# Kernel tuning notes

Measured on AMD Instinct MI355X. Metric: run time of the kernel, lower is better.

The kernel has to match this reference:

```python
import jax, jax.numpy as jnp
import numpy as np

B, N, C = 4, 2048, 1024
H = 16
D = C // H  # head_size = 64


def setup_inputs() -> dict:
    key = jax.random.key(0)
    ks = jax.random.split(key, 9)
    s = 1.0 / np.sqrt(C)
    return {
        "x": jax.random.normal(ks[0], (B, N, C), dtype=jnp.float32),
        "Wq": jax.random.normal(ks[1], (C, C), dtype=jnp.float32) * s,
        "bq": jnp.zeros((C,), dtype=jnp.float32),
        "Wk": jax.random.normal(ks[2], (C, C), dtype=jnp.float32) * s,
        "bk": jnp.zeros((C,), dtype=jnp.float32),
        "Wv": jax.random.normal(ks[3], (C, C), dtype=jnp.float32) * s,
        "bv": jnp.zeros((C,), dtype=jnp.float32),
        "Wo": jax.random.normal(ks[4], (C, C), dtype=jnp.float32) * s,
        "bo": jnp.zeros((C,), dtype=jnp.float32),
    }


def reference(x, Wq, bq, Wk, bk, Wv, bv, Wo, bo):
    scale = 1.0 / np.sqrt(D).astype(np.float32)
    # projections: [B,N,C] -> [B,H,N,D]
    def split_heads(t):
        return t.reshape(B, N, H, D).transpose(0, 2, 1, 3)
    q = split_heads(x @ Wq + bq)
    k = split_heads(x @ Wk + bk)
    v = split_heads(x @ Wv + bv)
    # scores: [B,H,N,N] -- full NxN materialized as in the original module
    attn = jnp.einsum("bhqd,bhkd->bhqk", q, k) * scale
    attn = jax.nn.softmax(attn, axis=-1)
    # context: [B,H,N,D] -> [B,N,C]
    ctx = jnp.einsum("bhqk,bhkd->bhqd", attn, v)
    ctx = ctx.transpose(0, 2, 1, 3).reshape(B, N, C)
    return ctx @ Wo + bo
```

## Files before the change

### kernel.cpp

```cpp
#include <hip/hip_runtime.h>
#include <hip/hip_bf16.h>

typedef __bf16 bf16_t;
typedef __bf16 bf16x4 __attribute__((ext_vector_type(4)));
typedef __bf16 bf16x8 __attribute__((ext_vector_type(8)));
typedef float f32x4 __attribute__((ext_vector_type(4)));
typedef unsigned int u32;

#define B_ 4
#define N_ 2048
#define C_ 1024
#define H_ 16
#define D_ 64

#define MFMA32(a, b, c) __builtin_amdgcn_mfma_f32_16x16x32_bf16((a), (b), (c), 0, 0, 0)

#if __has_builtin(__builtin_amdgcn_exp2f)
#define EXP2F(x) __builtin_amdgcn_exp2f(x)
#else
#define EXP2F(x) __expf((x) * 0.6931471805599453f)
#endif

#define QSCALE 0.18033688011112042f

__device__ __forceinline__ void async16(const bf16_t* g, bf16_t* l) {
    __builtin_amdgcn_global_load_lds(
        (const u32 __attribute__((address_space(1)))*)g,
        (u32 __attribute__((address_space(3)))*)l, 16, 0, 0);
}

#define SBAR()  asm volatile("s_barrier" ::: "memory")
#define VM6()   asm volatile("s_waitcnt vmcnt(6)" ::: "memory")
#define VM0()   asm volatile("s_waitcnt vmcnt(0)" ::: "memory")

__global__ __launch_bounds__(256)
void xconv_kernel(const float* __restrict__ x, bf16_t* __restrict__ xb)
{
    const size_t i = ((size_t)blockIdx.x * 256 + threadIdx.x) * 8;
    float4 a = *(const float4*)(x + i);
    float4 b = *(const float4*)(x + i + 4);
    bf16x8 o;
    o[0] = (bf16_t)a.x; o[1] = (bf16_t)a.y; o[2] = (bf16_t)a.z; o[3] = (bf16_t)a.w;
    o[4] = (bf16_t)b.x; o[5] = (bf16_t)b.y; o[6] = (bf16_t)b.z; o[7] = (bf16_t)b.w;
    *(bf16x8*)(xb + i) = o;
}

__global__ __launch_bounds__(256)
void wtrans_kernel(const float* __restrict__ W0, const float* __restrict__ W1,
                   const float* __restrict__ W2, const float* __restrict__ W3,
                   bf16_t* __restrict__ T0, bf16_t* __restrict__ T1,
                   bf16_t* __restrict__ T2, bf16_t* __restrict__ T3)
{
    const float* W; bf16_t* T;
    switch (blockIdx.z) {
        case 0:  W = W0; T = T0; break;
        case 1:  W = W1; T = T1; break;
        case 2:  W = W2; T = T2; break;
        default: W = W3; T = T3; break;
    }
    __shared__ bf16_t tile[64 * 72];
    const int tid = threadIdx.x;
    const int r0 = blockIdx.y * 64;
    const int c0 = blockIdx.x * 64;

    const int rr = tid >> 4;
    const int cc = (tid & 15) * 4;
    #pragma unroll
    for (int i = 0; i < 4; ++i) {
        const int row = rr + i * 16;
        float4 v = *(const float4*)(W + (size_t)(r0 + row) * C_ + c0 + cc);
        tile[(cc + 0) * 72 + row] = (bf16_t)v.x;
        tile[(cc + 1) * 72 + row] = (bf16_t)v.y;
        tile[(cc + 2) * 72 + row] = (bf16_t)v.z;
        tile[(cc + 3) * 72 + row] = (bf16_t)v.w;
    }
    __syncthreads();
    #pragma unroll
    for (int i = 0; i < 2; ++i) {
        const int ch = i * 256 + tid;
        const int n  = ch >> 3;
        const int k8 = (ch & 7) * 8;
        bf16x8 o = *(const bf16x8*)&tile[n * 72 + k8];
        *(bf16x8*)(T + (size_t)(c0 + n) * C_ + r0 + k8) = o;
    }
}

__device__ __forceinline__ void gemm128x256(const bf16_t* __restrict__ A,
                                            const bf16_t* __restrict__ Bt,
                                            bf16_t* smem, int m0, int n0,
                                            f32x4 (&acc)[4][4])
{
    const int tid  = threadIdx.x;
    const int w    = tid >> 6;
    const int lane = tid & 63;
    const int c    = lane & 15;
    const int quad = lane >> 4;
    const int wr   = w >> 2;
    const int wc   = w & 3;

    const int r0s = tid >> 2;
    const int kc  = (tid & 3) ^ ((r0s >> 1) & 3);
    const bf16_t* Ast0 = A  + (size_t)(m0 + r0s) * C_ + kc * 8;
    const bf16_t* Bst0 = Bt + (size_t)(n0 + r0s) * C_ + kc * 8;
    const bf16_t* Bst1 = Bt + (size_t)(n0 + r0s + 128) * C_ + kc * 8;

    const int xorc = (quad ^ ((c >> 1) & 3)) * 8;
    const bf16_t* Ard = smem + (wr * 64 + c) * 32 + xorc;
    const bf16_t* Brd = smem + 24576 + (wc * 64 + c) * 32 + xorc;
    bf16_t* sw = smem + w * 512;

    bf16x8 af[2][4], bfv[2][4];

#define STAGE6(BUF, KOFF) do { \
    async16(Ast0 + (KOFF),      sw + (BUF) * 8192); \
    async16(Ast0 + (KOFF) + 32, sw + (BUF) * 8192 + 4096); \
    async16(Bst0 + (KOFF),      sw + 24576 + (BUF) * 16384); \
    async16(Bst1 + (KOFF),      sw + 24576 + (BUF) * 16384 + 4096); \
    async16(Bst0 + (KOFF) + 32, sw + 24576 + (BUF) * 16384 + 8192); \
    async16(Bst1 + (KOFF) + 32, sw + 24576 + (BUF) * 16384 + 12288); } while (0)

#define LDFRAGS16(BUF) do { \
    _Pragma("unroll") \
    for (int ks = 0; ks < 2; ++ks) { \
        _Pragma("unroll") \
        for (int i = 0; i < 4; ++i) \
            af[ks][i]  = *(const bf16x8*)(Ard + (BUF) * 8192 + ks * 4096 + i * 512); \
        _Pragma("unroll") \
        for (int j = 0; j < 4; ++j) \
            bfv[ks][j] = *(const bf16x8*)(Brd + (BUF) * 16384 + ks * 8192 + j * 512); \
    } } while (0)

#define MFMA32ALL() do { \
    _Pragma("unroll") \
    for (int ks = 0; ks < 2; ++ks) \
        _Pragma("unroll") \
        for (int i = 0; i < 4; ++i) \
            _Pragma("unroll") \
            for (int j = 0; j < 4; ++j) \
                acc[i][j] = MFMA32(af[ks][i], bfv[ks][j], acc[i][j]); } while (0)

#define TILE(BUF, NXT, DOSTAGE, KOFF, VMK) do { \
    if (DOSTAGE) STAGE6(NXT, KOFF); \
    LDFRAGS16(BUF); \
    __builtin_amdgcn_s_setprio(1); MFMA32ALL(); __builtin_amdgcn_s_setprio(0); \
    VMK; \
    SBAR(); \
} while (0)

    STAGE6(0, 0);
    STAGE6(1, 64);
    VM6();
    SBAR();

    #pragma unroll 1
    for (int tt = 0; tt < 4; ++tt) {
        TILE(0, 2, 1, 128, VM6());
        TILE(1, 0, 1, 192, VM6());
        TILE(2, 1, 1, 256, VM6());
        Ast0 += 192; Bst0 += 192; Bst1 += 192;
    }
    TILE(0, 2, 1, 128, VM6());
    TILE(1, 0, 1, 192, VM6());
    TILE(2, 1, 0, 0,   VM0());
    TILE(0, 0, 0, 0,   ((void)0));

#undef TILE
#undef MFMA32ALL
#undef LDFRAGS16
#undef STAGE6
}

__global__ __launch_bounds__(512)
void gemm_qkv_kernel(const bf16_t* __restrict__ A, const bf16_t* __restrict__ Wt,
                     const float* __restrict__ bq, const float* __restrict__ bk,
                     const float* __restrict__ bv,
                     bf16_t* __restrict__ Qb, bf16_t* __restrict__ Kb,
                     bf16_t* __restrict__ Vtb)
{
    __shared__ bf16_t smem[73728];

    const int bid = blockIdx.x;
    const int x8  = bid & 7;
    const int ii  = bid >> 3;
    const int mb  = x8 * 8 + (ii & 7);
    const int nb  = ii >> 3;
    const int m0  = mb * 128, n0 = nb * 256;

    f32x4 acc[4][4] = {};
    gemm128x256(A, Wt, smem, m0, n0, acc);

    const int tid  = threadIdx.x;
    const int w    = tid >> 6;
    const int lane = tid & 63;
    const int c    = lane & 15;
    const int quad = lane >> 4;
    const int wr   = w >> 2;
    const int wc   = w & 3;

    const int which = n0 >> 10;
    const float* bias = (which == 0) ? bq : (which == 1) ? bk : bv;

    #pragma unroll
    for (int nf = 0; nf < 4; ++nf) {
        const int col  = n0 + wc * 64 + nf * 16 + c;
        const int ncol = col & 1023;
        const float bsf = bias[ncol];
        const int h = ncol >> 6, d = ncol & 63;
        #pragma unroll
        for (int mf = 0; mf < 4; ++mf) {
            const int rbase = m0 + wr * 64 + mf * 16 + quad * 4;
            if (which < 2) {
                bf16_t* out = which ? Kb : Qb;
                const float sc = which ? 1.0f : QSCALE;
                #pragma unroll
                for (int r = 0; r < 4; ++r) {
                    const int row = rbase + r;
                    const int bb = row >> 11, n = row & 2047;
                    out[(((size_t)bb * H_ + h) * N_ + n) * D_ + d] =
                        (bf16_t)((acc[mf][nf][r] + bsf) * sc);
                }
            } else {
                const int bb = rbase >> 11, nbv = rbase & 2047;
                bf16x4 o;
                #pragma unroll
                for (int r = 0; r < 4; ++r) o[r] = (bf16_t)(acc[mf][nf][r] + bsf);
                *(bf16x4*)(Vtb + (((size_t)bb * H_ + h) * D_ + d) * N_ + nbv) = o;
            }
        }
    }
}

__global__ __launch_bounds__(512)
void gemm_out_kernel(const bf16_t* __restrict__ A, const bf16_t* __restrict__ Bt,
                     const float* __restrict__ bias, float* __restrict__ out)
{
    __shared__ bf16_t smem[73728];

    const int bid = blockIdx.x;
    const int x8  = bid & 7;
    const int ii  = bid >> 3;
    const int mb  = x8 * 8 + (ii & 7);
    const int nb  = ii >> 3;
    const int m0  = mb * 128, n0 = nb * 256;

    f32x4 acc[4][4] = {};
    gemm128x256(A, Bt, smem, m0, n0, acc);

    const int tid  = threadIdx.x;
    const int w    = tid >> 6;
    const int lane = tid & 63;
    const int c    = lane & 15;
    const int quad = lane >> 4;
    const int wr   = w >> 2;
    const int wc   = w & 3;

    #pragma unroll
    for (int nf = 0; nf < 4; ++nf) {
        const int col   = n0 + wc * 64 + nf * 16 + c;
        const float bsf = bias[col];
        #pragma unroll
        for (int mf = 0; mf < 4; ++mf) {
            const int rbase = m0 + wr * 64 + mf * 16 + quad * 4;
            #pragma unroll
            for (int r = 0; r < 4; ++r)
                out[(size_t)(rbase + r) * C_ + col] = acc[mf][nf][r] + bsf;
        }
    }
}

__global__ __launch_bounds__(256, 2)
void attn_kernel(const bf16_t* __restrict__ Q, const bf16_t* __restrict__ K,
                 const bf16_t* __restrict__ Vt, bf16_t* __restrict__ ctx)
{
    __shared__ bf16_t ksh[64 * 64];
    __shared__ bf16_t vsh[64 * 64];

    const int tid  = threadIdx.x;
    const int w    = tid >> 6;
    const int lane = tid & 63;
    const int c    = lane & 15;
    const int quad = lane >> 4;

    const int bid   = blockIdx.x;
    const int bh    = (bid & 7) * 8 + ((bid >> 3) & 7);
    const int qtile = bid >> 6;
    const int b = bh >> 4, h = bh & 15;
    const size_t base = (size_t)bh * N_ * D_;
    const int qb = qtile * 256 + w * 64;

    bf16x8 qf[4][2];
    #pragma unroll
    for (int g = 0; g < 4; ++g)
        #pragma unroll
        for (int hh = 0; hh < 2; ++hh)
            qf[g][hh] = *(const bf16x8*)(Q + base + (size_t)(qb + g * 16 + c) * D_ + hh * 32 + quad * 8);

    bf16x8 ones;
    #pragma unroll
    for (int j = 0; j < 8; ++j) ones[j] = (bf16_t)1.0f;

    f32x4 O[4][4] = {};
    f32x4 O5[4] = {};

    for (int kt = 0; kt < N_; kt += 64) {
        __syncthreads();
        #pragma unroll
        for (int ph = 0; ph < 2; ++ph) {
            const int ch = ph * 256 + tid;
            const int rr = ch >> 3;
            const int e8 = ch & 7;
            const int sw = (e8 ^ (rr & 7)) * 8;
            bf16x8 kv = *(const bf16x8*)(K  + base + (size_t)(kt + rr) * D_ + e8 * 8);
            *(bf16x8*)&ksh[rr * 64 + sw] = kv;
            bf16x8 vv = *(const bf16x8*)(Vt + base + (size_t)rr * N_ + kt + e8 * 8);
            *(bf16x8*)&vsh[rr * 64 + sw] = vv;
        }
        __syncthreads();

        #pragma unroll
        for (int ss = 0; ss < 2; ++ss) {
            bf16x8 kb[2][2];
            #pragma unroll
            for (int s2 = 0; s2 < 2; ++s2) {
                const int key = (ss * 2 + s2) * 16 + c;
                #pragma unroll
                for (int hh = 0; hh < 2; ++hh)
                    kb[s2][hh] = *(const bf16x8*)&ksh[key * 64 + (((hh * 4 + quad) ^ (c & 7)) * 8)];
            }
            bf16x8 va[4];
            const int k8lo = ss * 4 + (quad >> 1);
            const int half = (quad & 1) * 4;
            #pragma unroll
            for (int df = 0; df < 4; ++df) {
                const int row = (df * 16 + c) * 64;
                bf16x4 lo = *(const bf16x4*)&vsh[row + ((k8lo       ^ (c & 7)) * 8) + half];
                bf16x4 hi = *(const bf16x4*)&vsh[row + (((k8lo + 2) ^ (c & 7)) * 8) + half];
                #pragma unroll
                for (int j = 0; j < 4; ++j) { va[df][j] = lo[j]; va[df][4 + j] = hi[j]; }
            }

            #pragma unroll
            for (int g = 0; g < 4; ++g) {
                f32x4 s0 = {}, s1 = {};
                s0 = MFMA32(kb[0][0], qf[g][0], s0);
                s0 = MFMA32(kb[0][1], qf[g][1], s0);
                s1 = MFMA32(kb[1][0], qf[g][0], s1);
                s1 = MFMA32(kb[1][1], qf[g][1], s1);

                bf16x8 pb;
                #pragma unroll
                for (int r = 0; r < 4; ++r) {
                    pb[r]     = (bf16_t)EXP2F(s0[r]);
                    pb[4 + r] = (bf16_t)EXP2F(s1[r]);
                }

                #pragma unroll
                for (int df = 0; df < 4; ++df)
                    O[g][df] = MFMA32(va[df], pb, O[g][df]);
                O5[g] = MFMA32(ones, pb, O5[g]);
            }
        }
    }

    #pragma unroll
    for (int g = 0; g < 4; ++g) {
        const float inv_l = 1.0f / O5[g][0];
        const int q = qb + g * 16 + c;
        #pragma unroll
        for (int df = 0; df < 4; ++df) {
            bf16x4 o;
            #pragma unroll
            for (int r = 0; r < 4; ++r) o[r] = (bf16_t)(O[g][df][r] * inv_l);
            *(bf16x4*)(ctx + ((size_t)b * N_ + q) * C_ + h * 64 + df * 16 + quad * 4) = o;
        }
    }
}

extern "C" void kernel_launch(void* const* d_in, const int* in_sizes, int n_in,
                              void* d_out, int out_size, void* d_ws, size_t ws_size,
                              hipStream_t stream) {
    const float* x  = (const float*)d_in[0];
    const float* Wq = (const float*)d_in[1];
    const float* bq = (const float*)d_in[2];
    const float* Wk = (const float*)d_in[3];
    const float* bk = (const float*)d_in[4];
    const float* Wv = (const float*)d_in[5];
    const float* bv = (const float*)d_in[6];
    const float* Wo = (const float*)d_in[7];
    const float* bo = (const float*)d_in[8];

    bf16_t* ws = (bf16_t*)d_ws;
    const size_t per = (size_t)B_ * N_ * C_;
    bf16_t* xb  = ws;
    bf16_t* ctx = ws;
    bf16_t* Qb  = ws + per;
    bf16_t* Kb  = ws + 2 * per;
    bf16_t* Vtb = ws + 3 * per;
    bf16_t* Wtqkv = ws + 4 * per;
    bf16_t* Wtq = Wtqkv;
    bf16_t* Wtk = Wtqkv + (size_t)C_ * C_;
    bf16_t* Wtv = Wtqkv + 2 * (size_t)C_ * C_;
    bf16_t* Wto = Wtqkv + 3 * (size_t)C_ * C_;

    dim3 blk(256);

    xconv_kernel<<<dim3(per / 2048), blk, 0, stream>>>(x, xb);
    wtrans_kernel<<<dim3(16, 16, 4), blk, 0, stream>>>(Wq, Wk, Wv, Wo, Wtq, Wtk, Wtv, Wto);

    gemm_qkv_kernel<<<dim3(768), dim3(512), 0, stream>>>(xb, Wtqkv, bq, bk, bv, Qb, Kb, Vtb);

    attn_kernel<<<dim3(512), blk, 0, stream>>>(Qb, Kb, Vtb, ctx);

    gemm_out_kernel<<<dim3(256), dim3(512), 0, stream>>>(ctx, Wto, bo, (float*)d_out);
}
```

Baseline: 252.1 us.

## Triple-buffer K/V tiles with async global-to-LDS loads in attention kernel

Replaces the synchronous per-tile K/V load into shared memory (two barriers per tile) with a three-stage ring buffer filled by global_load_lds async copies, so each tile's load overlaps the compute of earlier tiles and only one barrier per tile is needed. The row-sum MFMA against a ones vector is replaced by a scalar accumulation of the exponentials plus a cross-lane shuffle reduction at the end. MFMA sections are wrapped in s_setprio to favour matrix issue. LDS use grows to 48 KB per block, which may limit occupancy, and correctness depends on the hand-placed vmcnt waits and the unrolled loop covering all 32 tiles.

```diff
diff --git a/kernel.cpp b/kernel.cpp
--- a/kernel.cpp
+++ b/kernel.cpp
@@ -31,6 +31,7 @@
 
 #define SBAR()  asm volatile("s_barrier" ::: "memory")
 #define VM6()   asm volatile("s_waitcnt vmcnt(6)" ::: "memory")
+#define VM4()   asm volatile("s_waitcnt vmcnt(4)" ::: "memory")
 #define VM0()   asm volatile("s_waitcnt vmcnt(0)" ::: "memory")
 
 __global__ __launch_bounds__(256)
@@ -272,8 +273,7 @@
 void attn_kernel(const bf16_t* __restrict__ Q, const bf16_t* __restrict__ K,
                  const bf16_t* __restrict__ Vt, bf16_t* __restrict__ ctx)
 {
-    __shared__ bf16_t ksh[64 * 64];
-    __shared__ bf16_t vsh[64 * 64];
+    __shared__ bf16_t smem[24576];
 
     const int tid  = threadIdx.x;
     const int w    = tid >> 6;
@@ -288,6 +288,82 @@
     const size_t base = (size_t)bh * N_ * D_;
     const int qb = qtile * 256 + w * 64;
 
+    const int rs  = tid >> 3;
+    const int kcs = (tid & 7) ^ (rs & 7);
+    const bf16_t* Kst = K  + base + (size_t)rs * 64 + kcs * 8;
+    const bf16_t* Vst = Vt + base + (size_t)rs * 2048 + kcs * 8;
+    bf16_t* dstK = smem + w * 512;
+    bf16_t* dstV = smem + 12288 + w * 512;
+
+#define ASTAGE(NXT, T) do { \
+    async16(Kst + (T) * 4096,         dstK + (NXT) * 4096); \
+    async16(Kst + (T) * 4096 + 2048,  dstK + (NXT) * 4096 + 2048); \
+    async16(Vst + (T) * 64,           dstV + (NXT) * 4096); \
+    async16(Vst + (T) * 64 + 65536,   dstV + (NXT) * 4096 + 2048); } while (0)
+
+#define COMPUTE(BUF) do { \
+    const bf16_t* ksh = smem + (BUF) * 4096; \
+    const bf16_t* vsh = smem + 12288 + (BUF) * 4096; \
+    _Pragma("unroll") \
+    for (int ss = 0; ss < 2; ++ss) { \
+        bf16x8 kb[2][2]; \
+        _Pragma("unroll") \
+        for (int s2 = 0; s2 < 2; ++s2) { \
+            const int key = (ss * 2 + s2) * 16 + c; \
+            _Pragma("unroll") \
+            for (int hh = 0; hh < 2; ++hh) \
+                kb[s2][hh] = *(const bf16x8*)&ksh[key * 64 + (((hh * 4 + quad) ^ (c & 7)) * 8)]; \
+        } \
+        bf16x8 va[4]; \
+        const int k8lo = ss * 4 + (quad >> 1); \
+        const int half = (quad & 1) * 4; \
+        _Pragma("unroll") \
+        for (int df = 0; df < 4; ++df) { \
+            const int row = (df * 16 + c) * 64; \
+            bf16x4 lo = *(const bf16x4*)&vsh[row + ((k8lo       ^ (c & 7)) * 8) + half]; \
+            bf16x4 hi = *(const bf16x4*)&vsh[row + (((k8lo + 2) ^ (c & 7)) * 8) + half]; \
+            _Pragma("unroll") \
+            for (int j = 0; j < 4; ++j) { va[df][j] = lo[j]; va[df][4 + j] = hi[j]; } \
+        } \
+        _Pragma("unroll") \
+        for (int g = 0; g < 4; ++g) { \
+            f32x4 s0 = {}, s1 = {}; \
+            __builtin_amdgcn_s_setprio(1); \
+            s0 = MFMA32(kb[0][0], qf[g][0], s0); \
+            s0 = MFMA32(kb[0][1], qf[g][1], s0); \
+            s1 = MFMA32(kb[1][0], qf[g][0], s1); \
+            s1 = MFMA32(kb[1][1], qf[g][1], s1); \
+            __builtin_amdgcn_s_setprio(0); \
+            bf16x8 pb; \
+            float ls = 0.0f; \
+            _Pragma("unroll") \
+            for (int r = 0; r < 4; ++r) { \
+                const float e0 = EXP2F(s0[r]); \
+                const float e1 = EXP2F(s1[r]); \
+                pb[r]     = (bf16_t)e0; \
+                pb[4 + r] = (bf16_t)e1; \
+                ls += e0 + e1; \
+            } \
+            lsum[g] += ls; \
+            __builtin_amdgcn_s_setprio(1); \
+            _Pragma("unroll") \
+            for (int df = 0; df < 4; ++df) \
+                O[g][df] = MFMA32(va[df], pb, O[g][df]); \
+            __builtin_amdgcn_s_setprio(0); \
+        } \
+    } \
+} while (0)
+
+#define ATILE(BUF, NXT, DOSTAGE, TREL, VMK) do { \
+    if (DOSTAGE) ASTAGE(NXT, TREL); \
+    COMPUTE(BUF); \
+    VMK; \
+    SBAR(); \
+} while (0)
+
+    ASTAGE(0, 0);
+    ASTAGE(1, 1);
+
     bf16x8 qf[4][2];
     #pragma unroll
     for (int g = 0; g < 4; ++g)
@@ -295,76 +371,32 @@
         for (int hh = 0; hh < 2; ++hh)
             qf[g][hh] = *(const bf16x8*)(Q + base + (size_t)(qb + g * 16 + c) * D_ + hh * 32 + quad * 8);
 
-    bf16x8 ones;
-    #pragma unroll
-    for (int j = 0; j < 8; ++j) ones[j] = (bf16_t)1.0f;
-
     f32x4 O[4][4] = {};
-    f32x4 O5[4] = {};
-
-    for (int kt = 0; kt < N_; kt += 64) {
-        __syncthreads();
-        #pragma unroll
-        for (int ph = 0; ph < 2; ++ph) {
-            const int ch = ph * 256 + tid;
-            const int rr = ch >> 3;
-            const int e8 = ch & 7;
-            const int sw = (e8 ^ (rr & 7)) * 8;
-            bf16x8 kv = *(const bf16x8*)(K  + base + (size_t)(kt + rr) * D_ + e8 * 8);
-            *(bf16x8*)&ksh[rr * 64 + sw] = kv;
-            bf16x8 vv = *(const bf16x8*)(Vt + base + (size_t)rr * N_ + kt + e8 * 8);
-            *(bf16x8*)&vsh[rr * 64 + sw] = vv;
-        }
-        __syncthreads();
-
-        #pragma unroll
-        for (int ss = 0; ss < 2; ++ss) {
-            bf16x8 kb[2][2];
-            #pragma unroll
-            for (int s2 = 0; s2 < 2; ++s2) {
-                const int key = (ss * 2 + s2) * 16 + c;
-                #pragma unroll
-                for (int hh = 0; hh < 2; ++hh)
-                    kb[s2][hh] = *(const bf16x8*)&ksh[key * 64 + (((hh * 4 + quad) ^ (c & 7)) * 8)];
-            }
-            bf16x8 va[4];
-            const int k8lo = ss * 4 + (quad >> 1);
-            const int half = (quad & 1) * 4;
-            #pragma unroll
-            for (int df = 0; df < 4; ++df) {
-                const int row = (df * 16 + c) * 64;
-                bf16x4 lo = *(const bf16x4*)&vsh[row + ((k8lo       ^ (c & 7)) * 8) + half];
-                bf16x4 hi = *(const bf16x4*)&vsh[row + (((k8lo + 2) ^ (c & 7)) * 8) + half];
-                #pragma unroll
-                for (int j = 0; j < 4; ++j) { va[df][j] = lo[j]; va[df][4 + j] = hi[j]; }
-            }
-
-            #pragma unroll
-            for (int g = 0; g < 4; ++g) {
-                f32x4 s0 = {}, s1 = {};
-                s0 = MFMA32(kb[0][0], qf[g][0], s0);
-                s0 = MFMA32(kb[0][1], qf[g][1], s0);
-                s1 = MFMA32(kb[1][0], qf[g][0], s1);
-                s1 = MFMA32(kb[1][1], qf[g][1], s1);
-
-                bf16x8 pb;
-                #pragma unroll
-                for (int r = 0; r < 4; ++r) {
-                    pb[r]     = (bf16_t)EXP2F(s0[r]);
-                    pb[4 + r] = (bf16_t)EXP2F(s1[r]);
-                }
-
-                #pragma unroll
-                for (int df = 0; df < 4; ++df)
-                    O[g][df] = MFMA32(va[df], pb, O[g][df]);
-                O5[g] = MFMA32(ones, pb, O5[g]);
-            }
-        }
-    }
+    float lsum[4] = {};
+
+    VM4();
+    SBAR();
+
+    #pragma unroll 1
+    for (int it = 0; it < 10; ++it) {
+        ATILE(0, 2, 1, 2, VM4());
+        ATILE(1, 0, 1, 3, VM4());
+        ATILE(2, 1, 1, 4, VM4());
+        Kst += 12288; Vst += 192;
+    }
+    ATILE(0, 2, 0, 0, VM0());
+    ATILE(1, 0, 0, 0, ((void)0));
+
+#undef ATILE
+#undef COMPUTE
+#undef ASTAGE
 
     #pragma unroll
     for (int g = 0; g < 4; ++g) {
-        const float inv_l = 1.0f / O5[g][0];
+        float l = lsum[g];
+        l += __shfl_xor(l, 16);
+        l += __shfl_xor(l, 32);
+        const float inv_l = 1.0f / l;
         const int q = qb + g * 16 + c;
         #pragma unroll
         for (int df = 0; df < 4; ++df) {
```

Result: no change. 254.7 us (+1.0%).

## Load K/V fragments directly from global memory with register double-buffering

Applied to the files above, without the earlier changes.

Removes the shared-memory staging of K and V tiles and the two __syncthreads per 64-key tile in the attention kernel. Each wave now reads its K and Vt MFMA fragments straight from global memory into registers, alternating two register buffers so loads for the next 32-key step are issued while the current step computes. This trades shared-memory bandwidth and barriers for redundant global/L2 traffic, since all four waves fetch the same K/V data, and for higher register pressure.

```diff
diff --git a/kernel.cpp b/kernel.cpp
--- a/kernel.cpp
+++ b/kernel.cpp
@@ -268,13 +268,12 @@
     }
 }
 
+typedef union { bf16x8 v8; struct { bf16x4 lo; bf16x4 hi; } h; } vfrag_t;
+
 __global__ __launch_bounds__(256, 2)
 void attn_kernel(const bf16_t* __restrict__ Q, const bf16_t* __restrict__ K,
                  const bf16_t* __restrict__ Vt, bf16_t* __restrict__ ctx)
 {
-    __shared__ bf16_t ksh[64 * 64];
-    __shared__ bf16_t vsh[64 * 64];
-
     const int tid  = threadIdx.x;
     const int w    = tid >> 6;
     const int lane = tid & 63;
@@ -302,65 +301,61 @@
     f32x4 O[4][4] = {};
     f32x4 O5[4] = {};
 
-    for (int kt = 0; kt < N_; kt += 64) {
-        __syncthreads();
-        #pragma unroll
-        for (int ph = 0; ph < 2; ++ph) {
-            const int ch = ph * 256 + tid;
-            const int rr = ch >> 3;
-            const int e8 = ch & 7;
-            const int sw = (e8 ^ (rr & 7)) * 8;
-            bf16x8 kv = *(const bf16x8*)(K  + base + (size_t)(kt + rr) * D_ + e8 * 8);
-            *(bf16x8*)&ksh[rr * 64 + sw] = kv;
-            bf16x8 vv = *(const bf16x8*)(Vt + base + (size_t)rr * N_ + kt + e8 * 8);
-            *(bf16x8*)&vsh[rr * 64 + sw] = vv;
-        }
-        __syncthreads();
-
-        #pragma unroll
-        for (int ss = 0; ss < 2; ++ss) {
-            bf16x8 kb[2][2];
-            #pragma unroll
-            for (int s2 = 0; s2 < 2; ++s2) {
-                const int key = (ss * 2 + s2) * 16 + c;
-                #pragma unroll
-                for (int hh = 0; hh < 2; ++hh)
-                    kb[s2][hh] = *(const bf16x8*)&ksh[key * 64 + (((hh * 4 + quad) ^ (c & 7)) * 8)];
-            }
-            bf16x8 va[4];
-            const int k8lo = ss * 4 + (quad >> 1);
-            const int half = (quad & 1) * 4;
-            #pragma unroll
-            for (int df = 0; df < 4; ++df) {
-                const int row = (df * 16 + c) * 64;
-                bf16x4 lo = *(const bf16x4*)&vsh[row + ((k8lo       ^ (c & 7)) * 8) + half];
-                bf16x4 hi = *(const bf16x4*)&vsh[row + (((k8lo + 2) ^ (c & 7)) * 8) + half];
-                #pragma unroll
-                for (int j = 0; j < 4; ++j) { va[df][j] = lo[j]; va[df][4 + j] = hi[j]; }
-            }
-
-            #pragma unroll
-            for (int g = 0; g < 4; ++g) {
-                f32x4 s0 = {}, s1 = {};
-                s0 = MFMA32(kb[0][0], qf[g][0], s0);
-                s0 = MFMA32(kb[0][1], qf[g][1], s0);
-                s1 = MFMA32(kb[1][0], qf[g][0], s1);
-                s1 = MFMA32(kb[1][1], qf[g][1], s1);
-
-                bf16x8 pb;
-                #pragma unroll
-                for (int r = 0; r < 4; ++r) {
-                    pb[r]     = (bf16_t)EXP2F(s0[r]);
-                    pb[4 + r] = (bf16_t)EXP2F(s1[r]);
-                }
-
-                #pragma unroll
-                for (int df = 0; df < 4; ++df)
-                    O[g][df] = MFMA32(va[df], pb, O[g][df]);
-                O5[g] = MFMA32(ones, pb, O5[g]);
-            }
-        }
-    }
+    const bf16_t* Kp = K  + base + (size_t)c * 64 + quad * 8;
+    const bf16_t* Vp = Vt + base + (size_t)c * 2048
+                       + (quad >> 1) * 8 + (quad & 1) * 4;
+
+#define LOADF(KB, VA, S) do { \
+    _Pragma("unroll") \
+    for (int s2 = 0; s2 < 2; ++s2) \
+        _Pragma("unroll") \
+        for (int hh = 0; hh < 2; ++hh) \
+            KB[s2][hh] = *(const bf16x8*)(Kp + (size_t)(S) * 2048 + s2 * 1024 + hh * 32); \
+    _Pragma("unroll") \
+    for (int df = 0; df < 4; ++df) { \
+        VA[df].h.lo = *(const bf16x4*)(Vp + (size_t)df * 32768 + (S) * 32); \
+        VA[df].h.hi = *(const bf16x4*)(Vp + (size_t)df * 32768 + (S) * 32 + 16); \
+    } \
+} while (0)
+
+#define ACOMPUTE(KB, VA) do { \
+    _Pragma("unroll") \
+    for (int g = 0; g < 4; ++g) { \
+        f32x4 s0 = {}, s1 = {}; \
+        s0 = MFMA32(KB[0][0], qf[g][0], s0); \
+        s0 = MFMA32(KB[0][1], qf[g][1], s0); \
+        s1 = MFMA32(KB[1][0], qf[g][0], s1); \
+        s1 = MFMA32(KB[1][1], qf[g][1], s1); \
+        bf16x8 pb; \
+        _Pragma("unroll") \
+        for (int r = 0; r < 4; ++r) { \
+            pb[r]     = (bf16_t)EXP2F(s0[r]); \
+            pb[4 + r] = (bf16_t)EXP2F(s1[r]); \
+        } \
+        _Pragma("unroll") \
+        for (int df = 0; df < 4; ++df) \
+            O[g][df] = MFMA32(VA[df].v8, pb, O[g][df]); \
+        O5[g] = MFMA32(ones, pb, O5[g]); \
+    } \
+} while (0)
+
+    bf16x8 kbA[2][2], kbB[2][2];
+    vfrag_t vaA[4], vaB[4];
+
+    LOADF(kbA, vaA, 0);
+    #pragma unroll 1
+    for (int s = 0; s < 62; s += 2) {
+        LOADF(kbB, vaB, s + 1);
+        ACOMPUTE(kbA, vaA);
+        LOADF(kbA, vaA, s + 2);
+        ACOMPUTE(kbB, vaB);
+    }
+    LOADF(kbB, vaB, 63);
+    ACOMPUTE(kbA, vaA);
+    ACOMPUTE(kbB, vaB);
+
+#undef ACOMPUTE
+#undef LOADF
 
     #pragma unroll
     for (int g = 0; g < 4; ++g) {
```

After: 356.2 us. 41.3% more time.

## Double-buffer K/V tiles in attention kernel with one barrier per iteration

Applied to the files above, without the earlier changes.

Allocates two shared-memory buffers for the K and V tiles in the attention kernel. Each iteration now prefetches the next tile into the spare buffer right after the barrier and then computes on the current one, which removes one __syncthreads per key tile. The aim is to overlap global loads with the MFMA work. The cost is double the LDS footprint and a non-unrolled loop. The overlap depends on how the compiler schedules the register-staged loads, since each load must wait for its data before the LDS write.

```diff
diff --git a/kernel.cpp b/kernel.cpp
--- a/kernel.cpp
+++ b/kernel.cpp
@@ -272,8 +272,8 @@
 void attn_kernel(const bf16_t* __restrict__ Q, const bf16_t* __restrict__ K,
                  const bf16_t* __restrict__ Vt, bf16_t* __restrict__ ctx)
 {
-    __shared__ bf16_t ksh[64 * 64];
-    __shared__ bf16_t vsh[64 * 64];
+    __shared__ bf16_t ksh[2][64 * 64];
+    __shared__ bf16_t vsh[2][64 * 64];
 
     const int tid  = threadIdx.x;
     const int w    = tid >> 6;
@@ -302,20 +302,27 @@
     f32x4 O[4][4] = {};
     f32x4 O5[4] = {};
 
+#define ASTAGE(BUF, KT) do { \
+    _Pragma("unroll") \
+    for (int ph = 0; ph < 2; ++ph) { \
+        const int ch = ph * 256 + tid; \
+        const int rr = ch >> 3; \
+        const int e8 = ch & 7; \
+        const int sw = (e8 ^ (rr & 7)) * 8; \
+        bf16x8 kv = *(const bf16x8*)(K  + base + (size_t)((KT) + rr) * D_ + e8 * 8); \
+        *(bf16x8*)&ksh[BUF][rr * 64 + sw] = kv; \
+        bf16x8 vv = *(const bf16x8*)(Vt + base + (size_t)rr * N_ + (KT) + e8 * 8); \
+        *(bf16x8*)&vsh[BUF][rr * 64 + sw] = vv; \
+    } \
+} while (0)
+
+    ASTAGE(0, 0);
+
+    #pragma unroll 1
     for (int kt = 0; kt < N_; kt += 64) {
+        const int cur = (kt >> 6) & 1;
         __syncthreads();
-        #pragma unroll
-        for (int ph = 0; ph < 2; ++ph) {
-            const int ch = ph * 256 + tid;
-            const int rr = ch >> 3;
-            const int e8 = ch & 7;
-            const int sw = (e8 ^ (rr & 7)) * 8;
-            bf16x8 kv = *(const bf16x8*)(K  + base + (size_t)(kt + rr) * D_ + e8 * 8);
-            *(bf16x8*)&ksh[rr * 64 + sw] = kv;
-            bf16x8 vv = *(const bf16x8*)(Vt + base + (size_t)rr * N_ + kt + e8 * 8);
-            *(bf16x8*)&vsh[rr * 64 + sw] = vv;
-        }
-        __syncthreads();
+        if (kt + 64 < N_) ASTAGE(cur ^ 1, kt + 64);
 
         #pragma unroll
         for (int ss = 0; ss < 2; ++ss) {
@@ -325,7 +332,7 @@
                 const int key = (ss * 2 + s2) * 16 + c;
                 #pragma unroll
                 for (int hh = 0; hh < 2; ++hh)
-                    kb[s2][hh] = *(const bf16x8*)&ksh[key * 64 + (((hh * 4 + quad) ^ (c & 7)) * 8)];
+                    kb[s2][hh] = *(const bf16x8*)&ksh[cur][key * 64 + (((hh * 4 + quad) ^ (c & 7)) * 8)];
             }
             bf16x8 va[4];
             const int k8lo = ss * 4 + (quad >> 1);
@@ -333,8 +340,8 @@
             #pragma unroll
             for (int df = 0; df < 4; ++df) {
                 const int row = (df * 16 + c) * 64;
-                bf16x4 lo = *(const bf16x4*)&vsh[row + ((k8lo       ^ (c & 7)) * 8) + half];
-                bf16x4 hi = *(const bf16x4*)&vsh[row + (((k8lo + 2) ^ (c & 7)) * 8) + half];
+                bf16x4 lo = *(const bf16x4*)&vsh[cur][row + ((k8lo       ^ (c & 7)) * 8) + half];
+                bf16x4 hi = *(const bf16x4*)&vsh[cur][row + (((k8lo + 2) ^ (c & 7)) * 8) + half];
                 #pragma unroll
                 for (int j = 0; j < 4; ++j) { va[df][j] = lo[j]; va[df][4 + j] = hi[j]; }
             }
@@ -361,6 +368,8 @@
             }
         }
     }
+
+#undef ASTAGE
 
     #pragma unroll
     for (int g = 0; g < 4; ++g) {
```

Measured after the change: 254.6 us. No clear change (+1.0%).
